# Kernel optimization log

Hardware: AMD Instinct MI355X
Metric: run time of the kernel (lower is better)

The kernel has to match this reference:

```python
import jax, jax.numpy as jnp
import numpy as np
import math

NEG = -1e32
B, S, D, H, DFF, L = 16, 512, 1024, 8, 4096, 3
DK = D // H


def layernorm(x, g, b, eps=1e-5):
    mu = x.mean(-1, keepdims=True)
    var = ((x - mu) ** 2).mean(-1, keepdims=True)
    return (x - mu) / jnp.sqrt(var + eps) * g + b


def gen_dam(alphas, E, bmask):
    # alphas, E: [H, S, 2]; hard gumbel-softmax with straight-through
    Hh, Ss, _ = alphas.shape
    g = -jnp.log(E + 1e-5)
    y_soft = jax.nn.softmax(alphas + g, axis=-1)  # tau = 1
    idx = jnp.argmax(y_soft, axis=-1)
    y_hard = jax.nn.one_hot(idx, 2, dtype=y_soft.dtype)
    m = y_hard - jax.lax.stop_gradient(y_soft) + y_soft
    m = jnp.broadcast_to(m[:, :, 0:1], (Hh, Ss, Ss))
    m = jnp.triu(m)
    m = jnp.rot90(m, 1, axes=(1, 2))
    i = jnp.arange(Ss)[:, None]
    j = jnp.arange(Ss)[None, :]
    src = jnp.clip(j - i, 0, Ss - 1)
    shifted = m[:, jnp.arange(Ss)[:, None], src]  # mask_tri[:, i, j] = m[:, i, j - i]
    mask_tri = jnp.where(j >= i, shifted, 0.0)
    masks = mask_tri + jnp.swapaxes(jnp.triu(mask_tri, 1), 1, 2)
    masks = jnp.triu(masks, bmask)
    return masks


def attention(q, k, v, src_mask, dam, zero_pad, gammas):
    # q,k,v: [B,H,S,dk]; src_mask: [S,S] bool; dam: [H,S,S] bool
    dk = q.shape[-1]
    Ss = q.shape[2]
    scores = jnp.einsum('bhqd,bhkd->bhqk', q, k) / math.sqrt(dk)
    damb = dam[None]          # [1,H,S,S]
    smb = src_mask[None, None]  # [1,1,S,S]
    # NOTE: faithful to the torch code, where the first masked_fill(mask==0)
    # result is overwritten - only dam masks the first softmax.
    sc = jnp.where(damb, scores, NEG)
    sc = jax.nn.softmax(sc, axis=-1)
    sc = sc * smb.astype(sc.dtype) * damb.astype(sc.dtype)
    distcum = jnp.cumsum(sc, axis=-1)
    disttot = jnp.sum(sc, axis=-1, keepdims=True)
    pos = jnp.abs(jnp.arange(Ss)[None, :] - jnp.arange(Ss)[:, None]).astype(scores.dtype)
    dist = jnp.sqrt(jnp.clip((disttot - distcum) * pos[None, None], 0.0, None))
    dist = jax.lax.stop_gradient(dist)
    gamma = -jax.nn.softplus(gammas)[None]  # [1,H,1,1]
    te = jnp.clip(jnp.exp(dist * gamma), 1e-5, 1e5)
    scores = scores * te
    scores = jnp.where(smb, scores, NEG)
    scores = jnp.where(damb, scores, NEG)
    scores = jax.nn.softmax(scores, axis=-1)
    if zero_pad:
        scores = scores.at[:, :, 0, :].set(0.0)
    return jnp.einsum('bhqk,bhkd->bhqd', scores, v)


def transformer_layer(bmask, query, key, values, apply_pos, p):
    Bb, Ss, Dd = query.shape
    Hh = p['gammas'].shape[0]
    dam = gen_dam(p['alphas'], p['E'], bmask) == 0
    src_mask = jnp.triu(jnp.ones((Ss, Ss), jnp.int32), bmask) == 0
    k = (key @ p['kW'].T + p['kb']).reshape(Bb, Ss, Hh, -1).transpose(0, 2, 1, 3)
    q = (query @ p['kW'].T + p['kb']).reshape(Bb, Ss, Hh, -1).transpose(0, 2, 1, 3)  # kq_same
    v = (values @ p['vW'].T + p['vb']).reshape(Bb, Ss, Hh, -1).transpose(0, 2, 1, 3)
    att = attention(q, k, v, src_mask, dam, bmask == 0, p['gammas'])
    concat = att.transpose(0, 2, 1, 3).reshape(Bb, Ss, Dd)
    q2 = concat @ p['oW'].T + p['ob']
    x = layernorm(query + q2, p['ln1_g'], p['ln1_b'])
    if apply_pos:
        ff = jax.nn.relu(x @ p['w1'].T + p['b1']) @ p['w2'].T + p['b2']
        x = layernorm(x + ff, p['ln2_g'], p['ln2_b'])
    return x


def setup_inputs() -> dict:
    key = jax.random.key(0)
    ks = jax.random.split(key, 16)
    sc = 0.02
    return {
        'q_embed_data': jax.random.normal(ks[0], (B, S, D), jnp.float32),
        'qa_embed_data': jax.random.normal(ks[1], (B, S, D), jnp.float32),
        'kW': sc * jax.random.normal(ks[2], (L, D, D), jnp.float32),
        'kb': jnp.zeros((L, D), jnp.float32),
        'vW': sc * jax.random.normal(ks[3], (L, D, D), jnp.float32),
        'vb': jnp.zeros((L, D), jnp.float32),
        'oW': sc * jax.random.normal(ks[4], (L, D, D), jnp.float32),
        'ob': jnp.zeros((L, D), jnp.float32),
        'gammas': 0.5 * jax.random.normal(ks[5], (L, H, 1, 1), jnp.float32),
        'alphas': 0.001 * jax.random.normal(ks[6], (L, H, S, 2), jnp.float32),
        'ln1_g': jnp.ones((L, D), jnp.float32),
        'ln1_b': jnp.zeros((L, D), jnp.float32),
        'w1': sc * jax.random.normal(ks[7], (L, DFF, D), jnp.float32),
        'b1': jnp.zeros((L, DFF), jnp.float32),
        'w2': sc * jax.random.normal(ks[8], (L, D, DFF), jnp.float32),
        'b2': jnp.zeros((L, D), jnp.float32),
        'ln2_g': jnp.ones((L, D), jnp.float32),
        'ln2_b': jnp.zeros((L, D), jnp.float32),
        'gumbel_E': jax.random.exponential(ks[9], (L, H, S, 2), jnp.float32),
    }


def reference(q_embed_data, qa_embed_data, kW, kb, vW, vb, oW, ob, gammas,
              alphas, ln1_g, ln1_b, w1, b1, w2, b2, ln2_g, ln2_b, gumbel_E):
    def P(l):
        return {'kW': kW[l], 'kb': kb[l], 'vW': vW[l], 'vb': vb[l],
                'oW': oW[l], 'ob': ob[l], 'gammas': gammas[l], 'alphas': alphas[l],
                'ln1_g': ln1_g[l], 'ln1_b': ln1_b[l], 'w1': w1[l], 'b1': b1[l],
                'w2': w2[l], 'b2': b2[l], 'ln2_g': ln2_g[l], 'ln2_b': ln2_b[l],
                'E': gumbel_E[l]}
    # blocks_1: self-attention over answer embedding (mask=1)
    y = transformer_layer(1, qa_embed_data, qa_embed_data, qa_embed_data, True, P(0))
    # blocks_2: self-attn on question emb (no FFN), then cross-attn into y
    x = transformer_layer(1, q_embed_data, q_embed_data, q_embed_data, False, P(1))
    x = transformer_layer(0, x, x, y, True, P(2))
    return x
```

## Files before the change

### kernel.cpp

```cpp
#include <hip/hip_runtime.h>
#include <math.h>

#define NEGV -1e32f

typedef __bf16 bf16_t;
typedef _Float16 f16_t;
typedef __bf16 bf16x8 __attribute__((ext_vector_type(8)));
typedef __bf16 bf16x4 __attribute__((ext_vector_type(4)));
typedef _Float16 f16x8 __attribute__((ext_vector_type(8)));
typedef float floatx4 __attribute__((ext_vector_type(4)));

static __device__ __forceinline__ float fexp(float x) { return __expf(x); }
#if __has_builtin(__builtin_amdgcn_sqrtf)
static __device__ __forceinline__ float fsqrt(float x) { return __builtin_amdgcn_sqrtf(x); }
#else
static __device__ __forceinline__ float fsqrt(float x) { return sqrtf(x); }
#endif
#if __has_builtin(__builtin_amdgcn_rcpf)
static __device__ __forceinline__ float frcp(float x) { return __builtin_amdgcn_rcpf(x); }
#else
static __device__ __forceinline__ float frcp(float x) { return 1.0f / x; }
#endif

static __device__ __forceinline__ float wave_sum(float v) {
#pragma unroll
  for (int d = 32; d > 0; d >>= 1) v += __shfl_xor(v, d, 64);
  return v;
}
static __device__ __forceinline__ float wave_max(float v) {
#pragma unroll
  for (int d = 32; d > 0; d >>= 1) v = fmaxf(v, __shfl_xor(v, d, 64));
  return v;
}

static __device__ __forceinline__ void gl2lds16(const bf16_t* g, bf16_t* l) {
  __builtin_amdgcn_global_load_lds((__attribute__((address_space(1))) void*)(void*)g,
                                   (__attribute__((address_space(3))) void*)l, 16, 0, 0);
}

template <int WM, int WN, int FM, int FN, int BIAS_MODE, bool RELU, int OUT_MODE>
__global__ __launch_bounds__(WM * WN * 64) void gemm_db(
    const bf16_t* __restrict__ A, long lda, long a_so, long a_si,
    const bf16_t* __restrict__ B, long ldb, long b_so, long b_si,
    void* __restrict__ Cv, long ldc, long c_so, long c_si,
    const float* __restrict__ bias, int zdiv, int K, float alpha)
{
  constexpr int THREADS = WM * WN * 64;
  constexpr int BM = WM * FM * 16;
  constexpr int BN = WN * FN * 16;
  constexpr int RR = THREADS / 8;
  constexpr int RA = BM / RR;
  constexpr int RB = BN / RR;
  constexpr int NSTG = RA + RB;
  constexpr int MG = (FM >= 8) ? 2 : 1;
  constexpr int MSUB = FM / MG;
  constexpr int PH = 2 * MG;
  extern __shared__ bf16_t smem[];
  bf16_t* const Asb = smem;
  bf16_t* const Bsb = smem + 2 * (BM * 64);

  const int tid = threadIdx.x;
  const int wave = tid >> 6;
  const int lane = tid & 63;
  const int wm = wave / WN;
  const int wn = wave % WN;
  const int z = blockIdx.z;
  const long zo = z / zdiv;
  const long zi = z % zdiv;
  A += zo * a_so + zi * a_si;
  B += zo * b_so + zi * b_si;
  const long m0 = (long)blockIdx.x * BM;
  const long n0 = (long)blockIdx.y * BN;

  const int srow = tid >> 3;
  const int scol = ((tid & 7) ^ (srow & 7)) * 8;
  const bf16_t* gA = A + (m0 + srow) * lda + scol;
  const bf16_t* gB = B + (n0 + srow) * ldb + scol;
  const int lofs = wave * 512;

  floatx4 acc[FM][FN] = {};
  const int lr = lane & 15;
  const int kg = lane >> 4;
  const int NT = K >> 6;

  auto stage_round = [&](int q, long ko, int dstbuf) {
    if (q < RA)
      gl2lds16(gA + (long)(q * RR) * lda + ko,
               Asb + dstbuf * (BM * 64) + lofs + q * RR * 64);
    else
      gl2lds16(gB + (long)((q - RA) * RR) * ldb + ko,
               Bsb + dstbuf * (BN * 64) + lofs + (q - RA) * RR * 64);
  };

#pragma unroll
  for (int q = 0; q < NSTG; ++q) stage_round(q, 0, 0);

  for (int t = 0; t < NT; ++t) {
    const int buf = t & 1;
    const bool pf = (t + 1 < NT);
    const long ko = (long)(t + 1) * 64;
    if (pf) {
#pragma unroll
      for (int q = 0; q < 2; ++q) stage_round(q, ko, buf ^ 1);
      asm volatile("s_waitcnt vmcnt(2)" ::: "memory");
    } else {
      asm volatile("s_waitcnt vmcnt(0)" ::: "memory");
    }
    __builtin_amdgcn_s_barrier();
    __builtin_amdgcn_sched_barrier(0);
    const bf16_t* __restrict__ Ab = Asb + buf * (BM * 64);
    const bf16_t* __restrict__ Bb = Bsb + buf * (BN * 64);
#pragma unroll
    for (int h = 0; h < 2; ++h) {
      const int slot = ((h * 4 + kg) ^ (lr & 7)) * 8;
      bf16x8 bfr[FN];
#pragma unroll
      for (int g = 0; g < MG; ++g) {
        const int pi = h * MG + g;
        bf16x8 af[MSUB];
#pragma unroll
        for (int m = 0; m < MSUB; ++m)
          af[m] = *(const bf16x8*)(Ab + (wm * (FM * 16) + (g * MSUB + m) * 16 + lr) * 64 + slot);
        if (g == 0) {
#pragma unroll
          for (int n = 0; n < FN; ++n)
            bfr[n] = *(const bf16x8*)(Bb + (wn * (FN * 16) + n * 16 + lr) * 64 + slot);
        }
        if (pf) {
          const int q0 = 2 + pi * 6 / PH;
          const int q1 = 2 + (pi + 1) * 6 / PH;
#pragma unroll
          for (int q = q0; q < q1; ++q) stage_round(q, ko, buf ^ 1);
        }
        asm volatile("s_waitcnt lgkmcnt(0)" ::: "memory");
        __builtin_amdgcn_sched_barrier(0);
        __builtin_amdgcn_s_setprio(1);
#pragma unroll
        for (int m = 0; m < MSUB; ++m)
#pragma unroll
          for (int n = 0; n < FN; ++n)
            acc[g * MSUB + m][n] =
                __builtin_amdgcn_mfma_f32_16x16x32_bf16(af[m], bfr[n], acc[g * MSUB + m][n], 0, 0, 0);
        __builtin_amdgcn_s_setprio(0);
        __builtin_amdgcn_sched_barrier(0);
        __builtin_amdgcn_s_barrier();
      }
    }
  }

  const long coff = zo * c_so + zi * c_si;
  const int q4 = (lane >> 4) * 4;
#pragma unroll
  for (int m = 0; m < FM; ++m) {
#pragma unroll
    for (int n = 0; n < FN; ++n) {
#pragma unroll
      for (int r = 0; r < 4; ++r) {
        const long row = m0 + wm * (FM * 16) + m * 16 + q4 + r;
        const long col = n0 + wn * (FN * 16) + n * 16 + lr;
        float v = acc[m][n][r] * alpha;
        if (BIAS_MODE == 1) v += bias[col];
        if (BIAS_MODE == 2) v += bias[row];
        if (RELU) v = fmaxf(v, 0.0f);
        const long idx = coff + row * ldc + col;
        if (OUT_MODE == 1)      ((bf16_t*)Cv)[idx] = (bf16_t)v;
        else if (OUT_MODE == 2) ((f16_t*)Cv)[idx]  = (f16_t)v;
        else                    ((float*)Cv)[idx]  = v;
      }
    }
  }
}

__global__ __launch_bounds__(256) void attn_fused(
    const bf16_t* __restrict__ KQ,
    const bf16_t* __restrict__ VT,
    bf16_t* __restrict__ ATT,
    const int* __restrict__ bbit_l, const float* __restrict__ gam,
    const int bmask, const int zero_pad)
{
  extern __shared__ char sm[];
  f16_t*  Sp16 = (f16_t*)sm;
  bf16_t* SpB  = (bf16_t*)sm;
  bf16_t* AQ   = (bf16_t*)(sm + 33280);
  bf16_t* Bst  = (bf16_t*)(sm + 41472);

  const int tid = threadIdx.x;
  const int wave = tid >> 6;
  const int lane = tid & 63;
  const int lr = lane & 15;
  const int kg = lane >> 4;
  const int id = blockIdx.x;
  const int wg = (id & 7) * 256 + (id >> 3);
  const int bh = wg >> 4;
  const int qb = wg & 15;
  const int b = bh >> 3, h = bh & 7;
  const bf16_t* Qp = KQ + (long)b * 524288 + h * 128 + (long)qb * 32 * 1024;
  const bf16_t* Kp = KQ + (long)b * 524288 + h * 128;
  const bf16_t* Vp = VT + (long)b * 524288 + (long)h * 65536;

  const int srow = tid >> 3;
  const int scol = ((tid & 7) ^ (srow & 7)) * 8;
  const int lofs = wave * 512;

  gl2lds16(Qp + (long)srow * 1024 + scol,       AQ + lofs);
  gl2lds16(Qp + (long)srow * 1024 + 64 + scol,  AQ + 2048 + lofs);
#pragma unroll
  for (int r8 = 0; r8 < 8; ++r8)
    gl2lds16(Kp + (long)(r8 * 32 + srow) * 1024 + scol, Bst + r8 * 2048 + lofs);
  __syncthreads();

  floatx4 acc[2][8] = {};
#pragma unroll
  for (int step = 0; step < 4; ++step) {
    const int kt = step >> 1;
    const int hb = step & 1;
#pragma unroll
    for (int hh = 0; hh < 2; ++hh) {
      const int slot = ((hh * 4 + kg) ^ (lr & 7)) * 8;
      bf16x8 af[2], bfr[4];
#pragma unroll
      for (int m = 0; m < 2; ++m)
        af[m] = *(const bf16x8*)(AQ + kt * 2048 + (m * 16 + lr) * 64 + slot);
#pragma unroll
      for (int n = 0; n < 4; ++n)
        bfr[n] = *(const bf16x8*)(Bst + (wave * 64 + n * 16 + lr) * 64 + slot);
#pragma unroll
      for (int m = 0; m < 2; ++m)
#pragma unroll
        for (int n = 0; n < 4; ++n)
          acc[m][hb * 4 + n] =
              __builtin_amdgcn_mfma_f32_16x16x32_bf16(af[m], bfr[n], acc[m][hb * 4 + n], 0, 0, 0);
    }
    __syncthreads();
    if (step < 3) {
      const int kt2 = (step + 1) >> 1;
      const int hb2 = (step + 1) & 1;
#pragma unroll
      for (int r8 = 0; r8 < 8; ++r8)
        gl2lds16(Kp + (long)(hb2 * 256 + r8 * 32 + srow) * 1024 + kt2 * 64 + scol,
                 Bst + r8 * 2048 + lofs);
      __syncthreads();
    }
  }

  const int q4 = (lane >> 4) * 4;
#pragma unroll
  for (int m = 0; m < 2; ++m)
#pragma unroll
    for (int na = 0; na < 8; ++na)
#pragma unroll
      for (int rr = 0; rr < 4; ++rr) {
        const int row = m * 16 + q4 + rr;
        const int col = (na >> 2) * 256 + wave * 64 + (na & 3) * 16 + lr;
        Sp16[row * 520 + col] = (f16_t)(acc[m][na][rr] * 0.08838834764831845f);
      }
  __syncthreads();

#pragma unroll
  for (int r3 = 0; r3 < 4; ++r3)
    gl2lds16(Vp + (long)(r3 * 32 + srow) * 512 + scol, Bst + r3 * 2048 + lofs);

  {
    const float gamma = -log1pf(fexp(gam[h]));
    const int* bb = bbit_l + h * 512;
    const int jb = lane * 8;
#pragma unroll 1
    for (int rr8 = 0; rr8 < 8; ++rr8) {
      const int r = wave * 8 + rr8;
      const int i = qb * 32 + r;
      float sv[8];
      {
        const f16x8 a = *(const f16x8*)(Sp16 + r * 520 + jb);
#pragma unroll
        for (int u = 0; u < 8; ++u) sv[u] = (float)a[u];
      }
      float zz[8];
      bool band[8];
      float m1 = NEGV;
#pragma unroll
      for (int u = 0; u < 8; ++u) {
        const int j = jb + u;
        const bool bd = j < i + bmask;
        band[u] = bd;
        int d = j - i; d = d < 0 ? 0 : d;
        const bool allowed = bd || (bb[d] == 0);
        zz[u] = allowed ? sv[u] : NEGV;
        m1 = fmaxf(m1, zz[u]);
      }
      m1 = wave_max(m1);
      float e[8], es = 0.f;
#pragma unroll
      for (int u = 0; u < 8; ++u) { e[u] = fexp(zz[u] - m1); es += e[u]; }
      es = wave_sum(es);
      const float inv1 = frcp(es);
      float c[8];
      float run = 0.f;
#pragma unroll
      for (int u = 0; u < 8; ++u) {
        const float p = band[u] ? e[u] * inv1 : 0.f;
        run += p;
        c[u] = run;
      }
      float x = run;
#pragma unroll
      for (int d = 1; d < 64; d <<= 1) {
        const float y = __shfl_up(x, (unsigned)d, 64);
        if (lane >= d) x += y;
      }
      const float tot = __shfl(x, 63, 64);
      const float ex = x - run;
      float z2[8];
      float m2 = NEGV;
#pragma unroll
      for (int u = 0; u < 8; ++u) {
        const int j = jb + u;
        const float cc = c[u] + ex;
        const float pos = fabsf((float)(i - j));
        const float dist = fsqrt(fmaxf((tot - cc) * pos, 0.f));
        float te = fexp(dist * gamma);
        te = fminf(fmaxf(te, 1e-5f), 1e5f);
        z2[u] = band[u] ? sv[u] * te : NEGV;
        m2 = fmaxf(m2, z2[u]);
      }
      m2 = wave_max(m2);
      float f[8], es2 = 0.f;
#pragma unroll
      for (int u = 0; u < 8; ++u) { f[u] = fexp(z2[u] - m2); es2 += f[u]; }
      es2 = wave_sum(es2);
      const float inv2 = (zero_pad && i == 0) ? 0.f : frcp(es2);
      bf16x8 o;
#pragma unroll
      for (int u = 0; u < 8; ++u) o[u] = (bf16_t)(f[u] * inv2);
      *(bf16x8*)(SpB + r * 520 + jb) = o;
    }
  }
  __syncthreads();

  floatx4 acc2[2][2] = {};
  for (int kt = 0; kt < 8; ++kt) {
    const int buf = kt & 1;
    if (kt < 7) {
#pragma unroll
      for (int r3 = 0; r3 < 4; ++r3)
        gl2lds16(Vp + (long)(r3 * 32 + srow) * 512 + (kt + 1) * 64 + scol,
                 Bst + (buf ^ 1) * 8192 + r3 * 2048 + lofs);
      asm volatile("s_waitcnt vmcnt(4)" ::: "memory");
    } else {
      asm volatile("s_waitcnt vmcnt(0)" ::: "memory");
    }
    __builtin_amdgcn_s_barrier();
    __builtin_amdgcn_sched_barrier(0);
#pragma unroll
    for (int hh = 0; hh < 2; ++hh) {
      const int ks = hh * 4 + kg;
      bf16x8 af[2], bfr[2];
#pragma unroll
      for (int m = 0; m < 2; ++m)
        af[m] = *(const bf16x8*)(SpB + (m * 16 + lr) * 520 + kt * 64 + ks * 8);
#pragma unroll
      for (int n = 0; n < 2; ++n)
        bfr[n] = *(const bf16x8*)(Bst + buf * 8192 + (wave * 32 + n * 16 + lr) * 64 +
                                  (ks ^ (lr & 7)) * 8);
#pragma unroll
      for (int m = 0; m < 2; ++m)
#pragma unroll
        for (int n = 0; n < 2; ++n)
          acc2[m][n] = __builtin_amdgcn_mfma_f32_16x16x32_bf16(af[m], bfr[n], acc2[m][n], 0, 0, 0);
    }
    __builtin_amdgcn_sched_barrier(0);
    __builtin_amdgcn_s_barrier();
  }

#pragma unroll
  for (int m = 0; m < 2; ++m)
#pragma unroll
    for (int n = 0; n < 2; ++n)
#pragma unroll
      for (int rr = 0; rr < 4; ++rr) {
        const int row = m * 16 + q4 + rr;
        const int col = wave * 32 + n * 16 + lr;
        ATT[(long)b * 524288 + (long)(qb * 32 + row) * 1024 + h * 128 + col] =
            (bf16_t)acc2[m][n][rr];
      }
}

__global__ __launch_bounds__(256) void cast_kernel(const float* __restrict__ in,
                                                   bf16_t* __restrict__ out, long n)
{
  const long i = ((long)blockIdx.x * 256 + threadIdx.x) * 4;
  if (i >= n) return;
  const float4 v = *(const float4*)(in + i);
  bf16x4 o;
  o[0] = (bf16_t)v.x; o[1] = (bf16_t)v.y; o[2] = (bf16_t)v.z; o[3] = (bf16_t)v.w;
  *(bf16x4*)(out + i) = o;
}

__global__ void bbit_kernel(const float* __restrict__ alphas, const float* __restrict__ E,
                            int* __restrict__ bbit, int n)
{
  const int i = blockIdx.x * 256 + threadIdx.x;
  if (i >= n) return;
  const float l0 = alphas[2 * i]     - logf(E[2 * i]     + 1e-5f);
  const float l1 = alphas[2 * i + 1] - logf(E[2 * i + 1] + 1e-5f);
  bbit[i] = (l0 >= l1) ? 1 : 0;
}

template <bool XBF>
__global__ __launch_bounds__(256) void ln_kernel(
    const void* __restrict__ Xv, const float* __restrict__ R,
    const float* __restrict__ g, const float* __restrict__ b,
    float* __restrict__ out32, bf16_t* __restrict__ out16)
{
  const long row = blockIdx.x;
  const int t = threadIdx.x;
  float x0, x1, x2, x3;
  if (XBF) {
    const bf16x4 xv = *(const bf16x4*)((const bf16_t*)Xv + row * 1024 + t * 4);
    x0 = (float)xv[0]; x1 = (float)xv[1]; x2 = (float)xv[2]; x3 = (float)xv[3];
  } else {
    const float4 xv = *(const float4*)((const float*)Xv + row * 1024 + t * 4);
    x0 = xv.x; x1 = xv.y; x2 = xv.z; x3 = xv.w;
  }
  const float4 rv = *(const float4*)(R + row * 1024 + t * 4);
  const float v0 = x0 + rv.x, v1 = x1 + rv.y, v2 = x2 + rv.z, v3 = x3 + rv.w;
  float s  = v0 + v1 + v2 + v3;
  float s2 = v0 * v0 + v1 * v1 + v2 * v2 + v3 * v3;
  s = wave_sum(s); s2 = wave_sum(s2);
  __shared__ float red[8];
  const int wv = t >> 6, lane = t & 63;
  if (lane == 0) { red[wv] = s; red[4 + wv] = s2; }
  __syncthreads();
  s  = red[0] + red[1] + red[2] + red[3];
  s2 = red[4] + red[5] + red[6] + red[7];
  const float mu = s * (1.0f / 1024.0f);
  const float var = s2 * (1.0f / 1024.0f) - mu * mu;
  const float rstd = rsqrtf(var + 1e-5f);
  const float4 gv = *(const float4*)(g + t * 4);
  const float4 bv = *(const float4*)(b + t * 4);
  float4 ov;
  ov.x = (v0 - mu) * rstd * gv.x + bv.x;
  ov.y = (v1 - mu) * rstd * gv.y + bv.y;
  ov.z = (v2 - mu) * rstd * gv.z + bv.z;
  ov.w = (v3 - mu) * rstd * gv.w + bv.w;
  if (out32) *(float4*)(out32 + row * 1024 + t * 4) = ov;
  if (out16) {
    bf16x4 oh;
    oh[0] = (bf16_t)ov.x; oh[1] = (bf16_t)ov.y; oh[2] = (bf16_t)ov.z; oh[3] = (bf16_t)ov.w;
    *(bf16x4*)(out16 + row * 1024 + t * 4) = oh;
  }
}

extern "C" void kernel_launch(void* const* d_in, const int* in_sizes, int n_in,
                              void* d_out, int out_size, void* d_ws, size_t ws_size,
                              hipStream_t stream)
{
  (void)in_sizes; (void)n_in; (void)out_size; (void)ws_size;
  const float* q_emb  = (const float*)d_in[0];
  const float* qa_emb = (const float*)d_in[1];
  const float* kW = (const float*)d_in[2];
  const float* kb = (const float*)d_in[3];
  const float* vW = (const float*)d_in[4];
  const float* vb = (const float*)d_in[5];
  const float* oW = (const float*)d_in[6];
  const float* ob = (const float*)d_in[7];
  const float* gammas = (const float*)d_in[8];
  const float* alphas = (const float*)d_in[9];
  const float* ln1_g = (const float*)d_in[10];
  const float* ln1_b = (const float*)d_in[11];
  const float* w1 = (const float*)d_in[12];
  const float* b1 = (const float*)d_in[13];
  const float* w2 = (const float*)d_in[14];
  const float* b2 = (const float*)d_in[15];
  const float* ln2_g = (const float*)d_in[16];
  const float* ln2_b = (const float*)d_in[17];
  const float* gumE = (const float*)d_in[18];
  float* outp = (float*)d_out;

  static bool attr_done = false;
  if (!attr_done) {
    attr_done = true;
    (void)hipFuncSetAttribute(reinterpret_cast<const void*>(&gemm_db<2,2,4,4,1,false,1>),
                              hipFuncAttributeMaxDynamicSharedMemorySize, 65536);
    (void)hipFuncSetAttribute(reinterpret_cast<const void*>(&gemm_db<2,2,4,4,2,false,1>),
                              hipFuncAttributeMaxDynamicSharedMemorySize, 65536);
    (void)hipFuncSetAttribute(reinterpret_cast<const void*>(&gemm_db<2,2,4,4,1,false,0>),
                              hipFuncAttributeMaxDynamicSharedMemorySize, 65536);
    (void)hipFuncSetAttribute(reinterpret_cast<const void*>(&gemm_db<2,4,8,4,1,true,1>),
                              hipFuncAttributeMaxDynamicSharedMemorySize, 131072);
    (void)hipFuncSetAttribute(reinterpret_cast<const void*>(&attn_fused),
                              hipFuncAttributeMaxDynamicSharedMemorySize, 74240);
  }

  const size_t MBc = 1ull << 20;
  char* W = (char*)d_ws;
  int*    bbit = (int*)W;
  bf16_t* VB   = (bf16_t*)(W + 1 * MBc);
  bf16_t* XB   = (bf16_t*)(W + 17 * MBc);
  bf16_t* kWb  = (bf16_t*)(W + 33 * MBc);
  bf16_t* vWb  = (bf16_t*)(W + 39 * MBc);
  bf16_t* oWb  = (bf16_t*)(W + 45 * MBc);
  bf16_t* w1b  = (bf16_t*)(W + 51 * MBc);
  bf16_t* w2b  = (bf16_t*)(W + 59 * MBc);
  bf16_t* KQB  = (bf16_t*)(W + 67 * MBc);
  bf16_t* VT   = (bf16_t*)(W + 83 * MBc);
  bf16_t* ATT  = (bf16_t*)(W + 163 * MBc);
  float*  O32  = (float*)(W + 67 * MBc);
  bf16_t* X1B  = (bf16_t*)(W + 99 * MBc);
  bf16_t* H1B  = (bf16_t*)(W + 115 * MBc);

  const long ND = 8388608;

  auto run_layer = [&](int l, const void* Qin, bool qin_bf16, const bf16_t* XBp,
                       const bf16_t* VBp, bool apply_pos, int bmask,
                       float* o32, bf16_t* o16) {
    const bf16_t* kWl = kWb + (long)l * 1048576;
    const bf16_t* vWl = vWb + (long)l * 1048576;
    const bf16_t* oWl = oWb + (long)l * 1048576;
    gemm_db<2,2,4,4,1,false,1><<<dim3(64, 8, 1), dim3(256), 65536, stream>>>(
        XBp, 1024, 0, 0, kWl, 1024, 0, 0, (void*)KQB, 1024, 0, 0,
        kb + l * 1024, 1, 1024, 1.0f);
    gemm_db<2,2,4,4,2,false,1><<<dim3(8, 4, 16), dim3(256), 65536, stream>>>(
        vWl, 1024, 0, 0, VBp, 1024, 524288, 0, (void*)VT, 512, 524288, 0,
        vb + l * 1024, 1, 1024, 1.0f);
    const int zp = (bmask == 0) ? 1 : 0;
    attn_fused<<<dim3(2048), dim3(256), 74240, stream>>>(
        KQB, VT, ATT, bbit + l * 4096, gammas + l * 8, bmask, zp);
    gemm_db<2,2,4,4,1,false,0><<<dim3(64, 8, 1), dim3(256), 65536, stream>>>(
        ATT, 1024, 0, 0, oWl, 1024, 0, 0, (void*)O32, 1024, 0, 0,
        ob + l * 1024, 1, 1024, 1.0f);
    if (!apply_pos) {
      if (qin_bf16)
        ln_kernel<true><<<dim3(8192), dim3(256), 0, stream>>>(
            Qin, O32, ln1_g + l * 1024, ln1_b + l * 1024, o32, o16);
      else
        ln_kernel<false><<<dim3(8192), dim3(256), 0, stream>>>(
            Qin, O32, ln1_g + l * 1024, ln1_b + l * 1024, o32, o16);
    } else {
      cast_kernel<<<dim3(4096), dim3(256), 0, stream>>>(w1 + (long)l * 4194304, w1b, 4194304);
      cast_kernel<<<dim3(4096), dim3(256), 0, stream>>>(w2 + (long)l * 4194304, w2b, 4194304);
      if (qin_bf16)
        ln_kernel<true><<<dim3(8192), dim3(256), 0, stream>>>(
            Qin, O32, ln1_g + l * 1024, ln1_b + l * 1024, nullptr, X1B);
      else
        ln_kernel<false><<<dim3(8192), dim3(256), 0, stream>>>(
            Qin, O32, ln1_g + l * 1024, ln1_b + l * 1024, nullptr, X1B);
      gemm_db<2,4,8,4,1,true,1><<<dim3(32, 16, 1), dim3(512), 131072, stream>>>(
          X1B, 1024, 0, 0, w1b, 1024, 0, 0, (void*)H1B, 4096, 0, 0,
          b1 + l * 4096, 1, 1024, 1.0f);
      gemm_db<2,2,4,4,1,false,0><<<dim3(64, 8, 1), dim3(256), 65536, stream>>>(
          H1B, 4096, 0, 0, w2b, 4096, 0, 0, (void*)O32, 1024, 0, 0,
          b2 + l * 1024, 1, 4096, 1.0f);
      ln_kernel<true><<<dim3(8192), dim3(256), 0, stream>>>(
          X1B, O32, ln2_g + l * 1024, ln2_b + l * 1024, o32, o16);
    }
  };

  bbit_kernel<<<dim3(48), dim3(256), 0, stream>>>(alphas, gumE, bbit, 12288);
  cast_kernel<<<dim3(3072), dim3(256), 0, stream>>>(kW, kWb, 3145728);
  cast_kernel<<<dim3(3072), dim3(256), 0, stream>>>(vW, vWb, 3145728);
  cast_kernel<<<dim3(3072), dim3(256), 0, stream>>>(oW, oWb, 3145728);

  cast_kernel<<<dim3(8192), dim3(256), 0, stream>>>(qa_emb, XB, ND);
  run_layer(0, qa_emb, false, XB, XB, true, 1, nullptr, VB);
  cast_kernel<<<dim3(8192), dim3(256), 0, stream>>>(q_emb, XB, ND);
  run_layer(1, q_emb, false, XB, XB, false, 1, nullptr, XB);
  run_layer(2, XB, true, XB, VB, true, 0, outp, nullptr);
}
```

Before: 1.177 ms.

## Load attention operands straight from global memory to shrink LDS and raise occupancy

The fused attention kernel stops staging Q, K and V tiles through shared memory. MFMA fragments are now read directly from global memory, and only a 32x512 score buffer stays in LDS, using an XOR swizzle in place of the padded stride. Cutting LDS from about 74KB to 32KB per block, together with launch_bounds(256,3), is meant to let several blocks share a CU and drop the barriers. The cost is uncoalesced 16-byte global loads repeated across waves, which lean on L1/L2 bandwidth and latency hiding.

```diff
diff --git a/kernel.cpp b/kernel.cpp
--- a/kernel.cpp
+++ b/kernel.cpp
@@ -171,18 +171,15 @@
   }
 }
 
-__global__ __launch_bounds__(256) void attn_fused(
+__global__ __launch_bounds__(256, 3) void attn_fused(
     const bf16_t* __restrict__ KQ,
     const bf16_t* __restrict__ VT,
     bf16_t* __restrict__ ATT,
     const int* __restrict__ bbit_l, const float* __restrict__ gam,
     const int bmask, const int zero_pad)
 {
-  extern __shared__ char sm[];
-  f16_t*  Sp16 = (f16_t*)sm;
-  bf16_t* SpB  = (bf16_t*)sm;
-  bf16_t* AQ   = (bf16_t*)(sm + 33280);
-  bf16_t* Bst  = (bf16_t*)(sm + 41472);
+  __shared__ f16_t Sp16[32 * 512];
+  bf16_t* const SpB = (bf16_t*)Sp16;
 
   const int tid = threadIdx.x;
   const int wave = tid >> 6;
@@ -198,52 +195,39 @@
   const bf16_t* Kp = KQ + (long)b * 524288 + h * 128;
   const bf16_t* Vp = VT + (long)b * 524288 + (long)h * 65536;
 
-  const int srow = tid >> 3;
-  const int scol = ((tid & 7) ^ (srow & 7)) * 8;
-  const int lofs = wave * 512;
-
-  gl2lds16(Qp + (long)srow * 1024 + scol,       AQ + lofs);
-  gl2lds16(Qp + (long)srow * 1024 + 64 + scol,  AQ + 2048 + lofs);
-#pragma unroll
-  for (int r8 = 0; r8 < 8; ++r8)
-    gl2lds16(Kp + (long)(r8 * 32 + srow) * 1024 + scol, Bst + r8 * 2048 + lofs);
-  __syncthreads();
-
   floatx4 acc[2][8] = {};
+  bf16x8 aq[2][2][2];
+#pragma unroll
+  for (int kt = 0; kt < 2; ++kt)
+#pragma unroll
+    for (int hh = 0; hh < 2; ++hh)
+#pragma unroll
+      for (int m = 0; m < 2; ++m)
+        aq[kt][hh][m] =
+            *(const bf16x8*)(Qp + (long)(m * 16 + lr) * 1024 + kt * 64 + (hh * 4 + kg) * 8);
+
 #pragma unroll
   for (int step = 0; step < 4; ++step) {
     const int kt = step >> 1;
     const int hb = step & 1;
 #pragma unroll
     for (int hh = 0; hh < 2; ++hh) {
-      const int slot = ((hh * 4 + kg) ^ (lr & 7)) * 8;
-      bf16x8 af[2], bfr[4];
-#pragma unroll
-      for (int m = 0; m < 2; ++m)
-        af[m] = *(const bf16x8*)(AQ + kt * 2048 + (m * 16 + lr) * 64 + slot);
+      bf16x8 bfr[4];
 #pragma unroll
       for (int n = 0; n < 4; ++n)
-        bfr[n] = *(const bf16x8*)(Bst + (wave * 64 + n * 16 + lr) * 64 + slot);
+        bfr[n] = *(const bf16x8*)(Kp + (long)(hb * 256 + wave * 64 + n * 16 + lr) * 1024 +
+                                  kt * 64 + (hh * 4 + kg) * 8);
 #pragma unroll
       for (int m = 0; m < 2; ++m)
 #pragma unroll
         for (int n = 0; n < 4; ++n)
           acc[m][hb * 4 + n] =
-              __builtin_amdgcn_mfma_f32_16x16x32_bf16(af[m], bfr[n], acc[m][hb * 4 + n], 0, 0, 0);
-    }
-    __syncthreads();
-    if (step < 3) {
-      const int kt2 = (step + 1) >> 1;
-      const int hb2 = (step + 1) & 1;
-#pragma unroll
-      for (int r8 = 0; r8 < 8; ++r8)
-        gl2lds16(Kp + (long)(hb2 * 256 + r8 * 32 + srow) * 1024 + kt2 * 64 + scol,
-                 Bst + r8 * 2048 + lofs);
-      __syncthreads();
-    }
-  }
-
-  const int q4 = (lane >> 4) * 4;
+              __builtin_amdgcn_mfma_f32_16x16x32_bf16(aq[kt][hh][m], bfr[n], acc[m][hb * 4 + n], 0, 0, 0);
+    }
+    __builtin_amdgcn_sched_barrier(0);
+  }
+
+  const int q4 = kg * 4;
 #pragma unroll
   for (int m = 0; m < 2; ++m)
 #pragma unroll
@@ -252,25 +236,23 @@
       for (int rr = 0; rr < 4; ++rr) {
         const int row = m * 16 + q4 + rr;
         const int col = (na >> 2) * 256 + wave * 64 + (na & 3) * 16 + lr;
-        Sp16[row * 520 + col] = (f16_t)(acc[m][na][rr] * 0.08838834764831845f);
+        const int g = (col >> 3) ^ (row & 7);
+        Sp16[row * 512 + g * 8 + (col & 7)] = (f16_t)(acc[m][na][rr] * 0.08838834764831845f);
       }
   __syncthreads();
-
-#pragma unroll
-  for (int r3 = 0; r3 < 4; ++r3)
-    gl2lds16(Vp + (long)(r3 * 32 + srow) * 512 + scol, Bst + r3 * 2048 + lofs);
 
   {
     const float gamma = -log1pf(fexp(gam[h]));
     const int* bb = bbit_l + h * 512;
-    const int jb = lane * 8;
 #pragma unroll 1
     for (int rr8 = 0; rr8 < 8; ++rr8) {
       const int r = wave * 8 + rr8;
       const int i = qb * 32 + r;
+      const int jb = lane * 8;
+      const int ga = r * 512 + ((lane ^ (r & 7)) << 3);
       float sv[8];
       {
-        const f16x8 a = *(const f16x8*)(Sp16 + r * 520 + jb);
+        const f16x8 a = *(const f16x8*)(Sp16 + ga);
 #pragma unroll
         for (int u = 0; u < 8; ++u) sv[u] = (float)a[u];
       }
@@ -331,44 +313,34 @@
       bf16x8 o;
 #pragma unroll
       for (int u = 0; u < 8; ++u) o[u] = (bf16_t)(f[u] * inv2);
-      *(bf16x8*)(SpB + r * 520 + jb) = o;
+      *(bf16x8*)(SpB + ga) = o;
     }
   }
   __syncthreads();
 
   floatx4 acc2[2][2] = {};
+#pragma unroll 1
   for (int kt = 0; kt < 8; ++kt) {
-    const int buf = kt & 1;
-    if (kt < 7) {
-#pragma unroll
-      for (int r3 = 0; r3 < 4; ++r3)
-        gl2lds16(Vp + (long)(r3 * 32 + srow) * 512 + (kt + 1) * 64 + scol,
-                 Bst + (buf ^ 1) * 8192 + r3 * 2048 + lofs);
-      asm volatile("s_waitcnt vmcnt(4)" ::: "memory");
-    } else {
-      asm volatile("s_waitcnt vmcnt(0)" ::: "memory");
-    }
-    __builtin_amdgcn_s_barrier();
-    __builtin_amdgcn_sched_barrier(0);
 #pragma unroll
     for (int hh = 0; hh < 2; ++hh) {
       const int ks = hh * 4 + kg;
       bf16x8 af[2], bfr[2];
 #pragma unroll
-      for (int m = 0; m < 2; ++m)
-        af[m] = *(const bf16x8*)(SpB + (m * 16 + lr) * 520 + kt * 64 + ks * 8);
+      for (int m = 0; m < 2; ++m) {
+        const int row = m * 16 + lr;
+        const int g = (kt * 8 + ks) ^ (lr & 7);
+        af[m] = *(const bf16x8*)(SpB + row * 512 + g * 8);
+      }
 #pragma unroll
       for (int n = 0; n < 2; ++n)
-        bfr[n] = *(const bf16x8*)(Bst + buf * 8192 + (wave * 32 + n * 16 + lr) * 64 +
-                                  (ks ^ (lr & 7)) * 8);
+        bfr[n] = *(const bf16x8*)(Vp + (long)(wave * 32 + n * 16 + lr) * 512 +
+                                  kt * 64 + ks * 8);
 #pragma unroll
       for (int m = 0; m < 2; ++m)
 #pragma unroll
         for (int n = 0; n < 2; ++n)
           acc2[m][n] = __builtin_amdgcn_mfma_f32_16x16x32_bf16(af[m], bfr[n], acc2[m][n], 0, 0, 0);
     }
-    __builtin_amdgcn_sched_barrier(0);
-    __builtin_amdgcn_s_barrier();
   }
 
 #pragma unroll
@@ -487,8 +459,6 @@
                               hipFuncAttributeMaxDynamicSharedMemorySize, 65536);
     (void)hipFuncSetAttribute(reinterpret_cast<const void*>(&gemm_db<2,4,8,4,1,true,1>),
                               hipFuncAttributeMaxDynamicSharedMemorySize, 131072);
-    (void)hipFuncSetAttribute(reinterpret_cast<const void*>(&attn_fused),
-                              hipFuncAttributeMaxDynamicSharedMemorySize, 74240);
   }
 
   const size_t MBc = 1ull << 20;
@@ -523,7 +493,7 @@
         vWl, 1024, 0, 0, VBp, 1024, 524288, 0, (void*)VT, 512, 524288, 0,
         vb + l * 1024, 1, 1024, 1.0f);
     const int zp = (bmask == 0) ? 1 : 0;
-    attn_fused<<<dim3(2048), dim3(256), 74240, stream>>>(
+    attn_fused<<<dim3(2048), dim3(256), 0, stream>>>(
         KQB, VT, ATT, bbit + l * 4096, gammas + l * 8, bmask, zp);
     gemm_db<2,2,4,4,1,false,0><<<dim3(64, 8, 1), dim3(256), 65536, stream>>>(
         ATT, 1024, 0, 0, oWl, 1024, 0, 0, (void*)O32, 1024, 0, 0,
```

Measured after the change: 1.173 ms. Within noise of the previous version (-0.3%).
